# Optimization experiments

Measured on AMD Instinct MI355X. Metric: run time of the kernel, lower is better.

## Reference

```python
import jax, jax.numpy as jnp
import numpy as np

B = 2
E = [16384, 32768, 65536, 131072]
CONVS = [256, 128, 64, 32, 8]


def mesh_conv(x, gemm, W, b):
    # x: (B, C, E); gemm: (E, 4) neighbor edge indices; W: (Cout, Cin, 5)
    n = x[:, :, gemm]  # (B, C, E, 4) irregular gather over mesh topology
    f1, f2, f3, f4 = n[..., 0], n[..., 1], n[..., 2], n[..., 3]
    # MeshCNN symmetric functions over the 4 gemm neighbors
    G = jnp.stack([x, f1 + f3, f2 + f4, jnp.abs(f1 - f3), jnp.abs(f2 - f4)], axis=-1)  # (B,C,E,5)
    return jnp.einsum('bces,ocs->boe', G, W) + b[None, :, None]


def inorm(x, eps=1e-5):
    # InstanceNorm2d, affine=False: normalize per (sample, channel) over edge dim
    m = jnp.mean(x, axis=2, keepdims=True)
    v = jnp.var(x, axis=2, keepdims=True)
    return (x - m) * jax.lax.rsqrt(v + eps)


def setup_inputs() -> dict:
    key = jax.random.key(0)
    ks = iter(jax.random.split(key, 64))
    inp = {}
    inp['fe'] = jax.random.normal(next(ks), (B, CONVS[0], E[0]), jnp.float32)
    for i in range(3):
        inp[f'skip{i}'] = jax.random.normal(next(ks), (B, CONVS[i + 1], E[i + 1]), jnp.float32)
    for r in range(4):
        inp[f'gemm{r}'] = jax.random.randint(next(ks), (E[r], 4), 0, E[r], jnp.int32)
    for i in range(3):
        inp[f'unpool{i}'] = jax.random.randint(next(ks), (E[i + 1],), 0, E[i], jnp.int32)

    def mk(cout, cin, name):
        inp[f'W{name}'] = jax.random.normal(next(ks), (cout, cin, 5), jnp.float32) * (1.0 / np.sqrt(5.0 * cin))
        inp[f'b{name}'] = jnp.zeros((cout,), jnp.float32)

    for i in range(3):
        mk(CONVS[i + 1], CONVS[i], f'up{i}')
        mk(CONVS[i + 1], CONVS[i + 1], f'c{i}')
    mk(CONVS[4], CONVS[3], 'upf')
    mk(CONVS[4], CONVS[4], 'cf')
    return inp


def reference(fe, skip0, skip1, skip2, gemm0, gemm1, gemm2, gemm3,
              unpool0, unpool1, unpool2,
              Wup0, bup0, Wc0, bc0, Wup1, bup1, Wc1, bc1, Wup2, bup2, Wc2, bc2,
              Wupf, bupf, Wcf, bcf):
    gemms = [gemm0, gemm1, gemm2, gemm3]
    unpools = [unpool0, unpool1, unpool2]
    skips = [skip0, skip1, skip2]
    Wups = [Wup0, Wup1, Wup2]
    bups = [bup0, bup1, bup2]
    Wcs = [Wc0, Wc1, Wc2]
    bcs = [bc0, bc1, bc2]
    x = fe
    for i in range(3):  # fixed small loop over decoder stages
        x1 = mesh_conv(x, gemms[i], Wups[i], bups[i])      # up_conv at coarse res
        x1 = x1[:, :, unpools[i]]                          # MeshUnpool: copy to fine edges
        x1 = x1 + skips[i]                                 # transfer_data skip add
        x1 = mesh_conv(x1, gemms[i + 1], Wcs[i], bcs[i])   # conv1 at fine res
        x = jax.nn.relu(inorm(x1))                         # InstanceNorm + ReLU (blocks=0)
    # final UpConv: no unroll, no skip
    x1 = mesh_conv(x, gemms[3], Wupf, bupf)
    x1 = mesh_conv(x1, gemms[3], Wcf, bcf)
    return jax.nn.relu(inorm(x1))
```

## Files before the change

### kernel.cpp

```cpp
#include <hip/hip_runtime.h>
#include <hip/hip_bf16.h>
#include <cstdint>
#include <cstddef>


typedef short s16x8 __attribute__((ext_vector_type(8)));
typedef unsigned short u16x8 __attribute__((ext_vector_type(8)));
typedef float f32x4 __attribute__((ext_vector_type(4)));

__device__ __forceinline__ float bfbits2f(unsigned short u) {
    unsigned int x = ((unsigned int)u) << 16;
    float f; __builtin_memcpy(&f, &x, sizeof(f)); return f;
}
__device__ __forceinline__ unsigned short f2bfbits(float f) {
    __hip_bfloat16 h = __float2bfloat16(f);
    unsigned short u; __builtin_memcpy(&u, &h, sizeof(u)); return u;
}

__global__ __launch_bounds__(256) void k_transpose_in(
    const float* __restrict__ in, unsigned short* __restrict__ out, int C, int E)
{
    __shared__ float tile[64][65];
    const int e0 = blockIdx.x * 64;
    const int c0 = blockIdx.y * 64;
    const int b  = blockIdx.z;
    const float* inb = in + (size_t)b * C * E;
    const int l = threadIdx.x % 64;
    const int g = threadIdx.x / 64;
#pragma unroll
    for (int i = 0; i < 16; ++i) {
        const int c = i * 4 + g;
        tile[c][l] = inb[(size_t)(c0 + c) * E + e0 + l];
    }
    __syncthreads();
    unsigned short* outb = out + (size_t)b * E * C;
#pragma unroll
    for (int i = 0; i < 16; ++i) {
        const int e = i * 4 + g;
        outb[(size_t)(e0 + e) * C + c0 + l] = f2bfbits(tile[l][e]);
    }
}

__global__ __launch_bounds__(256) void k_prep_b(
    const float* __restrict__ W, unsigned short* __restrict__ Bp, int C, int O)
{
    const int p = blockIdx.x * 256 + threadIdx.x;
    const int total = 5 * C * O;
    if (p >= total) return;
    const int j = p & 7;
    const int t = p >> 3;
    const int o = t % O;
    const int kk = t / O;
    const int k = kk * 8 + j;
    const int s = k / C;
    const int c = k - s * C;
    Bp[p] = f2bfbits(W[((size_t)o * C + c) * 5 + s]);
}

__global__ __launch_bounds__(256) void k_prep_w(
    const float* __restrict__ W, float* __restrict__ Wt, int C, int O)
{
    const int idx = blockIdx.x * 256 + threadIdx.x;
    const int total = C * 5 * O;
    if (idx >= total) return;
    const int k = idx / O;
    const int o = idx % O;
    const int c = k / 5;
    const int s = k - 5 * c;
    Wt[idx] = W[((size_t)o * C + c) * 5 + s];
}

template<int C, int O, bool STATS>
__global__ __launch_bounds__(256) void k_conv_mfma(
    const unsigned short* __restrict__ x, const int* __restrict__ gm,
    const unsigned short* __restrict__ Bp, const float* __restrict__ bias,
    unsigned short* __restrict__ out, float* __restrict__ stats, int E)
{
    constexpr int NT  = O / 16;
    constexpr int ITS = C / 32;
    static_assert(C % 32 == 0 && O % 16 == 0, "bad cfg");
    const int tid  = threadIdx.x;
    const int wave = tid >> 6;
    const int lane = tid & 63;
    const int m    = lane & 15;
    const int kq   = lane >> 4;
    const int b    = blockIdx.y;
    const int e    = blockIdx.x * 64 + wave * 16 + m;
    const unsigned short* xb = x + (size_t)b * E * C;

    const int4 gi = *reinterpret_cast<const int4*>(gm + 4 * (size_t)e);
    const unsigned short* p0  = xb + (size_t)e * C;
    const unsigned short* pf1 = xb + (size_t)gi.x * C;
    const unsigned short* pf2 = xb + (size_t)gi.y * C;
    const unsigned short* pf3 = xb + (size_t)gi.z * C;
    const unsigned short* pf4 = xb + (size_t)gi.w * C;

    const s16x8* Bp8 = reinterpret_cast<const s16x8*>(Bp);

    f32x4 acc[NT];
#pragma unroll
    for (int nt = 0; nt < NT; ++nt) acc[nt] = (f32x4){0.f, 0.f, 0.f, 0.f};

#pragma unroll
    for (int s = 0; s < 5; ++s) {
        const unsigned short* pa = (s == 0) ? p0 : ((s == 1 || s == 3) ? pf1 : pf2);
        const unsigned short* pb = (s == 0) ? p0 : ((s == 1 || s == 3) ? pf3 : pf4);
        for (int it = 0; it < ITS; ++it) {
            const int c0 = it * 32 + kq * 8;
            s16x8 afrag;
            if (s == 0) {
                afrag = *reinterpret_cast<const s16x8*>(pa + c0);
            } else {
                const s16x8 av = *reinterpret_cast<const s16x8*>(pa + c0);
                const s16x8 bv = *reinterpret_cast<const s16x8*>(pb + c0);
#pragma unroll
                for (int j = 0; j < 8; ++j) {
                    const float fa = bfbits2f((unsigned short)av[j]);
                    const float fb = bfbits2f((unsigned short)bv[j]);
                    const float t = (s < 3) ? (fa + fb) : fabsf(fa - fb);
                    afrag[j] = (short)f2bfbits(t);
                }
            }
            const int kk = s * (C / 8) + it * 4 + kq;
#pragma unroll
            for (int nt = 0; nt < NT; ++nt) {
                const s16x8 bfrag = Bp8[(size_t)kk * O + nt * 16 + m];
                acc[nt] = __builtin_amdgcn_mfma_f32_16x16x32_bf16(afrag, bfrag, acc[nt], 0, 0, 0);
            }
        }
    }

    const int ebase = blockIdx.x * 64 + wave * 16 + kq * 4;
    float ssum[NT], ssq[NT];
#pragma unroll
    for (int nt = 0; nt < NT; ++nt) {
        const int o = nt * 16 + m;
        const float bo = bias[o];
        float s = 0.f, q = 0.f;
#pragma unroll
        for (int r = 0; r < 4; ++r) {
            const float z = acc[nt][r] + bo;
            out[((size_t)b * E + (ebase + r)) * O + o] = f2bfbits(z);
            s += z; q += z * z;
        }
        ssum[nt] = s; ssq[nt] = q;
    }

    if constexpr (STATS) {
        __shared__ float ls[4][2][O];
#pragma unroll
        for (int nt = 0; nt < NT; ++nt) {
            float s = ssum[nt], q = ssq[nt];
            s += __shfl_xor(s, 16); s += __shfl_xor(s, 32);
            q += __shfl_xor(q, 16); q += __shfl_xor(q, 32);
            if (kq == 0) { ls[wave][0][nt * 16 + m] = s; ls[wave][1][nt * 16 + m] = q; }
        }
        __syncthreads();
        if (tid < O) {
            const float S = ls[0][0][tid] + ls[1][0][tid] + ls[2][0][tid] + ls[3][0][tid];
            const float Q = ls[0][1][tid] + ls[1][1][tid] + ls[2][1][tid] + ls[3][1][tid];
            atomicAdd(&stats[((size_t)b * O + tid) * 2], S);
            atomicAdd(&stats[((size_t)b * O + tid) * 2 + 1], Q);
        }
    }
}

template<int C, int O, bool STATS>
__global__ __launch_bounds__(256) void k_conv_small(
    const unsigned short* __restrict__ x, const int* __restrict__ gm,
    const float* __restrict__ Wt, const float* __restrict__ bias,
    unsigned short* __restrict__ out, float* __restrict__ stats, int E)
{
    static_assert(O == 8 && C % 8 == 0, "bad cfg");
    __shared__ float ls[2 * O];
    const int tid = threadIdx.x;
    if constexpr (STATS) {
        if (tid < 2 * O) ls[tid] = 0.f;
        __syncthreads();
    }
    const int b = blockIdx.y;
    const int e = blockIdx.x * 256 + tid;
    const unsigned short* xb = x + (size_t)b * E * C;
    const int4 gi = *reinterpret_cast<const int4*>(gm + 4 * (size_t)e);
    const unsigned short* rp[5] = {
        xb + (size_t)e * C, xb + (size_t)gi.x * C, xb + (size_t)gi.y * C,
        xb + (size_t)gi.z * C, xb + (size_t)gi.w * C };

    float acc[O];
#pragma unroll
    for (int o = 0; o < O; ++o) acc[o] = bias[o];

#pragma unroll
    for (int c = 0; c < C; c += 8) {
        u16x8 rv[5];
#pragma unroll
        for (int k = 0; k < 5; ++k) rv[k] = *reinterpret_cast<const u16x8*>(rp[k] + c);
#pragma unroll
        for (int cc = 0; cc < 8; ++cc) {
            const float x0 = bfbits2f(rv[0][cc]);
            const float f1 = bfbits2f(rv[1][cc]);
            const float f2 = bfbits2f(rv[2][cc]);
            const float f3 = bfbits2f(rv[3][cc]);
            const float f4 = bfbits2f(rv[4][cc]);
            const float gv[5] = { x0, f1 + f3, f2 + f4, fabsf(f1 - f3), fabsf(f2 - f4) };
            const float* wbase = Wt + (size_t)(c + cc) * 5 * O;
#pragma unroll
            for (int s = 0; s < 5; ++s)
#pragma unroll
                for (int o = 0; o < O; ++o)
                    acc[o] += gv[s] * wbase[s * O + o];
        }
    }

    u16x8 ov;
#pragma unroll
    for (int o = 0; o < O; ++o) ov[o] = f2bfbits(acc[o]);
    *reinterpret_cast<u16x8*>(out + ((size_t)b * E + e) * O) = ov;

    if constexpr (STATS) {
#pragma unroll
        for (int o = 0; o < O; ++o) {
            atomicAdd(&ls[o * 2], acc[o]);
            atomicAdd(&ls[o * 2 + 1], acc[o] * acc[o]);
        }
        __syncthreads();
        if (tid < 2 * O) atomicAdd(&stats[(size_t)b * 2 * O + tid], ls[tid]);
    }
}

template<int O>
__global__ __launch_bounds__(256) void k_unpool_skip(
    const unsigned short* __restrict__ y, const int* __restrict__ up,
    const float* __restrict__ skip, unsigned short* __restrict__ out,
    int Ein, int Eout)
{
    __shared__ float sk[O][65];
    const int b  = blockIdx.y;
    const int e0 = blockIdx.x * 64;
    const int t  = threadIdx.x;
    constexpr int L = O / 16;
#pragma unroll
    for (int i = 0; i < L; ++i) {
        const int flat = i * 256 + t;
        const int o = flat >> 4;
        const int el4 = (flat & 15) * 4;
        const float4 v = *reinterpret_cast<const float4*>(
            skip + ((size_t)b * O + o) * Eout + e0 + el4);
        sk[o][el4]     = v.x;
        sk[o][el4 + 1] = v.y;
        sk[o][el4 + 2] = v.z;
        sk[o][el4 + 3] = v.w;
    }
    __syncthreads();
    constexpr int OG  = O / 4;
    constexpr int EPP = 256 / OG;
    const int o4  = (t % OG) * 4;
    const int elg = t / OG;
#pragma unroll
    for (int p = 0; p < 64 / EPP; ++p) {
        const int el = p * EPP + elg;
        const int e  = e0 + el;
        const int u  = up[e];
        const ushort4 yv = *reinterpret_cast<const ushort4*>(
            y + ((size_t)b * Ein + u) * O + o4);
        ushort4 ov;
        ov.x = f2bfbits(bfbits2f(yv.x) + sk[o4 + 0][el]);
        ov.y = f2bfbits(bfbits2f(yv.y) + sk[o4 + 1][el]);
        ov.z = f2bfbits(bfbits2f(yv.z) + sk[o4 + 2][el]);
        ov.w = f2bfbits(bfbits2f(yv.w) + sk[o4 + 3][el]);
        *reinterpret_cast<ushort4*>(out + ((size_t)b * Eout + e) * O + o4) = ov;
    }
}

__global__ __launch_bounds__(256) void k_scale(
    const float* __restrict__ stats, float* __restrict__ ss, int BC, float invE)
{
    const int t = threadIdx.x;
    if (t < BC) {
        const float sum = stats[t * 2];
        const float sq  = stats[t * 2 + 1];
        const float m   = sum * invE;
        const float var = fmaxf(sq * invE - m * m, 0.f);
        const float sc  = rsqrtf(var + 1e-5f);
        ss[t * 2] = sc;
        ss[t * 2 + 1] = -m * sc;
    }
}

template<int C>
__global__ __launch_bounds__(256) void k_norm_relu(
    unsigned short* __restrict__ x, const float* __restrict__ ss, int E)
{
    const int b = blockIdx.y;
    const size_t i8 = ((size_t)blockIdx.x * 256 + threadIdx.x) * 8;
    const int c0 = (int)(i8 % C);
    unsigned short* p = x + (size_t)b * E * C + i8;
    const u16x8 v = *reinterpret_cast<const u16x8*>(p);
    u16x8 r;
#pragma unroll
    for (int j = 0; j < 8; ++j) {
        const float sc = ss[(b * C + c0 + j) * 2];
        const float sh = ss[(b * C + c0 + j) * 2 + 1];
        r[j] = f2bfbits(fmaxf(bfbits2f(v[j]) * sc + sh, 0.f));
    }
    *reinterpret_cast<u16x8*>(p) = r;
}

__global__ __launch_bounds__(256) void k_final_out(
    const unsigned short* __restrict__ z, const float* __restrict__ ss,
    float* __restrict__ out, int E)
{
    const int b = blockIdx.y;
    const int idx = blockIdx.x * 256 + threadIdx.x;
    const int o = idx / E;
    const int e = idx % E;
    const float sc = ss[((size_t)b * 8 + o) * 2];
    const float sh = ss[((size_t)b * 8 + o) * 2 + 1];
    const float v = bfbits2f(z[((size_t)b * E + e) * 8 + o]) * sc + sh;
    out[(size_t)b * 8 * E + idx] = fmaxf(v, 0.f);
}

extern "C" void kernel_launch(void* const* d_in, const int* in_sizes, int n_in,
                              void* d_out, int out_size, void* d_ws, size_t ws_size,
                              hipStream_t stream)
{
    (void)in_sizes; (void)n_in; (void)out_size; (void)ws_size;

    const float* fe = (const float*)d_in[0];
    const int* gemm0 = (const int*)d_in[4];
    const int* gemm1 = (const int*)d_in[5];
    const int* gemm2 = (const int*)d_in[6];
    const int* gemm3 = (const int*)d_in[7];
    const int* up0 = (const int*)d_in[8];
    const int* up1 = (const int*)d_in[9];
    const int* up2 = (const int*)d_in[10];
    const float* bup0 = (const float*)d_in[12];
    const float* bc0  = (const float*)d_in[14];
    const float* bup1 = (const float*)d_in[16];
    const float* bc1  = (const float*)d_in[18];
    const float* bup2 = (const float*)d_in[20];
    const float* bc2  = (const float*)d_in[22];
    const float* bupf = (const float*)d_in[24];
    const float* bcf  = (const float*)d_in[26];

    unsigned short* wsb = (unsigned short*)d_ws;
    const size_t NP = 8388608;
    unsigned short* P0 = wsb;
    unsigned short* P1 = wsb + NP;
    unsigned short* P2 = wsb + 2 * NP;
    unsigned short* Bp_up0 = wsb + 3 * NP;
    unsigned short* Bp_c0  = Bp_up0 + 163840;
    unsigned short* Bp_up1 = Bp_c0  + 81920;
    unsigned short* Bp_c1  = Bp_up1 + 40960;
    unsigned short* Bp_up2 = Bp_c1  + 20480;
    unsigned short* Bp_c2  = Bp_up2 + 10240;
    float* fls    = (float*)(Bp_c2 + 5120);
    float* wt_upf = fls;
    float* wt_cf  = wt_upf + 1280;
    float* stats0 = wt_cf  + 320;
    float* stats1 = stats0 + 512;
    float* stats2 = stats1 + 256;
    float* stats3 = stats2 + 128;
    float* ss0    = stats3 + 32;
    float* ss1    = ss0 + 512;
    float* ss2    = ss1 + 256;
    float* ss3    = ss2 + 128;

    hipMemsetAsync(stats0, 0, 928 * sizeof(float), stream);

    const dim3 blk(256);

    k_transpose_in<<<dim3(16384 / 64, 256 / 64, 2), blk, 0, stream>>>(fe, P0, 256, 16384);

    k_prep_b<<<dim3(163840 / 256), blk, 0, stream>>>((const float*)d_in[11], Bp_up0, 256, 128);
    k_prep_b<<<dim3(81920 / 256),  blk, 0, stream>>>((const float*)d_in[13], Bp_c0, 128, 128);
    k_prep_b<<<dim3(40960 / 256),  blk, 0, stream>>>((const float*)d_in[15], Bp_up1, 128, 64);
    k_prep_b<<<dim3(20480 / 256),  blk, 0, stream>>>((const float*)d_in[17], Bp_c1, 64, 64);
    k_prep_b<<<dim3(10240 / 256),  blk, 0, stream>>>((const float*)d_in[19], Bp_up2, 64, 32);
    k_prep_b<<<dim3(5120 / 256),   blk, 0, stream>>>((const float*)d_in[21], Bp_c2, 32, 32);
    k_prep_w<<<dim3((1280 + 255) / 256), blk, 0, stream>>>((const float*)d_in[23], wt_upf, 32, 8);
    k_prep_w<<<dim3((320 + 255) / 256),  blk, 0, stream>>>((const float*)d_in[25], wt_cf, 8, 8);

    k_conv_mfma<256, 128, false><<<dim3(16384 / 64, 2), blk, 0, stream>>>(P0, gemm0, Bp_up0, bup0, P1, nullptr, 16384);
    k_unpool_skip<128><<<dim3(32768 / 64, 2), blk, 0, stream>>>(P1, up0, (const float*)d_in[1], P2, 16384, 32768);
    k_conv_mfma<128, 128, true><<<dim3(32768 / 64, 2), blk, 0, stream>>>(P2, gemm1, Bp_c0, bc0, P0, stats0, 32768);
    k_scale<<<dim3(1), blk, 0, stream>>>(stats0, ss0, 256, 1.f / 32768.f);
    k_norm_relu<128><<<dim3(32768 * 128 / 2048, 2), blk, 0, stream>>>(P0, ss0, 32768);

    k_conv_mfma<128, 64, false><<<dim3(32768 / 64, 2), blk, 0, stream>>>(P0, gemm1, Bp_up1, bup1, P1, nullptr, 32768);
    k_unpool_skip<64><<<dim3(65536 / 64, 2), blk, 0, stream>>>(P1, up1, (const float*)d_in[2], P2, 32768, 65536);
    k_conv_mfma<64, 64, true><<<dim3(65536 / 64, 2), blk, 0, stream>>>(P2, gemm2, Bp_c1, bc1, P0, stats1, 65536);
    k_scale<<<dim3(1), blk, 0, stream>>>(stats1, ss1, 128, 1.f / 65536.f);
    k_norm_relu<64><<<dim3(65536 * 64 / 2048, 2), blk, 0, stream>>>(P0, ss1, 65536);

    k_conv_mfma<64, 32, false><<<dim3(65536 / 64, 2), blk, 0, stream>>>(P0, gemm2, Bp_up2, bup2, P1, nullptr, 65536);
    k_unpool_skip<32><<<dim3(131072 / 64, 2), blk, 0, stream>>>(P1, up2, (const float*)d_in[3], P2, 65536, 131072);
    k_conv_mfma<32, 32, true><<<dim3(131072 / 64, 2), blk, 0, stream>>>(P2, gemm3, Bp_c2, bc2, P0, stats2, 131072);
    k_scale<<<dim3(1), blk, 0, stream>>>(stats2, ss2, 64, 1.f / 131072.f);
    k_norm_relu<32><<<dim3(131072 * 32 / 2048, 2), blk, 0, stream>>>(P0, ss2, 131072);

    k_conv_small<32, 8, false><<<dim3(131072 / 256, 2), blk, 0, stream>>>(P0, gemm3, wt_upf, bupf, P1, nullptr, 131072);
    k_conv_small<8, 8, true><<<dim3(131072 / 256, 2), blk, 0, stream>>>(P1, gemm3, wt_cf, bcf, P2, stats3, 131072);
    k_scale<<<dim3(1), blk, 0, stream>>>(stats3, ss3, 16, 1.f / 131072.f);
    k_final_out<<<dim3(8 * 131072 / 256, 2), blk, 0, stream>>>(P2, ss3, (float*)d_out, 131072);
}
```

Measured before the change: 785.7 us.

## Stage gathered neighbor features in LDS and route final up-conv through MFMA

The MFMA conv kernel now loads the 64-edge tile's gather indices into shared memory and has all threads cooperatively gather neighbor rows into an LDS tile. For C<=128 it builds the sum and abs-difference terms for each neighbor pair in one pass, so each gathered row is read from global memory once instead of twice and the A fragments are read from LDS. The final 32->8 up-conv moves from the scalar small-channel kernel to the MFMA kernel, with output channels zero-padded to 16 and only 8 written. The cost is extra syncthreads, LDS pressure that may lower occupancy, and wasted MFMA work on the padded channels.

```diff
diff --git a/kernel.cpp b/kernel.cpp
--- a/kernel.cpp
+++ b/kernel.cpp
@@ -42,19 +42,19 @@
 }
 
 __global__ __launch_bounds__(256) void k_prep_b(
-    const float* __restrict__ W, unsigned short* __restrict__ Bp, int C, int O)
+    const float* __restrict__ W, unsigned short* __restrict__ Bp, int C, int OP, int OL)
 {
     const int p = blockIdx.x * 256 + threadIdx.x;
-    const int total = 5 * C * O;
+    const int total = 5 * C * OP;
     if (p >= total) return;
     const int j = p & 7;
     const int t = p >> 3;
-    const int o = t % O;
-    const int kk = t / O;
+    const int o = t % OP;
+    const int kk = t / OP;
     const int k = kk * 8 + j;
     const int s = k / C;
     const int c = k - s * C;
-    Bp[p] = f2bfbits(W[((size_t)o * C + c) * 5 + s]);
+    Bp[p] = (o < OL) ? f2bfbits(W[((size_t)o * C + c) * 5 + s]) : (unsigned short)0;
 }
 
 __global__ __launch_bounds__(256) void k_prep_w(
@@ -70,80 +70,162 @@
     Wt[idx] = W[((size_t)o * C + c) * 5 + s];
 }
 
-template<int C, int O, bool STATS>
+template<int C, int O, bool STATS, int OW = O>
 __global__ __launch_bounds__(256) void k_conv_mfma(
     const unsigned short* __restrict__ x, const int* __restrict__ gm,
     const unsigned short* __restrict__ Bp, const float* __restrict__ bias,
     unsigned short* __restrict__ out, float* __restrict__ stats, int E)
 {
-    constexpr int NT  = O / 16;
-    constexpr int ITS = C / 32;
+    constexpr int NT    = O / 16;
+    constexpr int ITS   = C / 32;
+    constexpr int OCT   = C / 8;
+    constexpr int ITERS = (64 * OCT) / 256;
+    constexpr int PAD   = 8;
+    constexpr int RW    = C + PAD;
+    constexpr bool PAIRED = (C <= 128);
+    constexpr int SLOTS = PAIRED ? 2 : 1;
     static_assert(C % 32 == 0 && O % 16 == 0, "bad cfg");
+
+    __shared__ unsigned short smem[SLOTS][64][RW];
+    __shared__ int gis[64][4];
+
     const int tid  = threadIdx.x;
     const int wave = tid >> 6;
     const int lane = tid & 63;
     const int m    = lane & 15;
     const int kq   = lane >> 4;
     const int b    = blockIdx.y;
-    const int e    = blockIdx.x * 64 + wave * 16 + m;
+    const int e0   = blockIdx.x * 64;
     const unsigned short* xb = x + (size_t)b * E * C;
-
-    const int4 gi = *reinterpret_cast<const int4*>(gm + 4 * (size_t)e);
-    const unsigned short* p0  = xb + (size_t)e * C;
-    const unsigned short* pf1 = xb + (size_t)gi.x * C;
-    const unsigned short* pf2 = xb + (size_t)gi.y * C;
-    const unsigned short* pf3 = xb + (size_t)gi.z * C;
-    const unsigned short* pf4 = xb + (size_t)gi.w * C;
-
     const s16x8* Bp8 = reinterpret_cast<const s16x8*>(Bp);
 
+    if (tid < 64)
+        *reinterpret_cast<int4*>(gis[tid]) =
+            *reinterpret_cast<const int4*>(gm + 4 * (size_t)(e0 + tid));
+
     f32x4 acc[NT];
 #pragma unroll
     for (int nt = 0; nt < NT; ++nt) acc[nt] = (f32x4){0.f, 0.f, 0.f, 0.f};
 
-#pragma unroll
-    for (int s = 0; s < 5; ++s) {
-        const unsigned short* pa = (s == 0) ? p0 : ((s == 1 || s == 3) ? pf1 : pf2);
-        const unsigned short* pb = (s == 0) ? p0 : ((s == 1 || s == 3) ? pf3 : pf4);
+    auto mfma_seg = [&](int slot, int s) {
+#pragma unroll
         for (int it = 0; it < ITS; ++it) {
-            const int c0 = it * 32 + kq * 8;
-            s16x8 afrag;
-            if (s == 0) {
-                afrag = *reinterpret_cast<const s16x8*>(pa + c0);
-            } else {
-                const s16x8 av = *reinterpret_cast<const s16x8*>(pa + c0);
-                const s16x8 bv = *reinterpret_cast<const s16x8*>(pb + c0);
-#pragma unroll
-                for (int j = 0; j < 8; ++j) {
-                    const float fa = bfbits2f((unsigned short)av[j]);
-                    const float fb = bfbits2f((unsigned short)bv[j]);
-                    const float t = (s < 3) ? (fa + fb) : fabsf(fa - fb);
-                    afrag[j] = (short)f2bfbits(t);
-                }
-            }
-            const int kk = s * (C / 8) + it * 4 + kq;
+            const s16x8 afrag = *reinterpret_cast<const s16x8*>(
+                &smem[slot][wave * 16 + m][it * 32 + kq * 8]);
+            const int kkb = s * OCT + it * 4 + kq;
 #pragma unroll
             for (int nt = 0; nt < NT; ++nt) {
-                const s16x8 bfrag = Bp8[(size_t)kk * O + nt * 16 + m];
+                const s16x8 bfrag = Bp8[(size_t)kkb * O + nt * 16 + m];
                 acc[nt] = __builtin_amdgcn_mfma_f32_16x16x32_bf16(afrag, bfrag, acc[nt], 0, 0, 0);
             }
         }
-    }
-
-    const int ebase = blockIdx.x * 64 + wave * 16 + kq * 4;
+    };
+
+#pragma unroll
+    for (int i = 0; i < ITERS; ++i) {
+        const int task = i * 256 + tid;
+        const int r    = task / OCT;
+        const int oct  = task % OCT;
+        const u16x8 v = *reinterpret_cast<const u16x8*>(
+            xb + (size_t)(e0 + r) * C + oct * 8);
+        *reinterpret_cast<u16x8*>(&smem[0][r][oct * 8]) = v;
+    }
+    __syncthreads();
+    mfma_seg(0, 0);
+    __syncthreads();
+
+    if constexpr (PAIRED) {
+#pragma unroll
+        for (int i = 0; i < ITERS; ++i) {
+            const int task = i * 256 + tid;
+            const int r    = task / OCT;
+            const int oct  = task % OCT;
+            const u16x8 a = *reinterpret_cast<const u16x8*>(
+                xb + (size_t)gis[r][0] * C + oct * 8);
+            const u16x8 c = *reinterpret_cast<const u16x8*>(
+                xb + (size_t)gis[r][2] * C + oct * 8);
+            u16x8 vs, vd;
+#pragma unroll
+            for (int j = 0; j < 8; ++j) {
+                const float fa = bfbits2f(a[j]);
+                const float fc = bfbits2f(c[j]);
+                vs[j] = f2bfbits(fa + fc);
+                vd[j] = f2bfbits(fabsf(fa - fc));
+            }
+            *reinterpret_cast<u16x8*>(&smem[0][r][oct * 8]) = vs;
+            *reinterpret_cast<u16x8*>(&smem[SLOTS - 1][r][oct * 8]) = vd;
+        }
+        __syncthreads();
+        mfma_seg(0, 1);
+        mfma_seg(SLOTS - 1, 3);
+        __syncthreads();
+#pragma unroll
+        for (int i = 0; i < ITERS; ++i) {
+            const int task = i * 256 + tid;
+            const int r    = task / OCT;
+            const int oct  = task % OCT;
+            const u16x8 a = *reinterpret_cast<const u16x8*>(
+                xb + (size_t)gis[r][1] * C + oct * 8);
+            const u16x8 c = *reinterpret_cast<const u16x8*>(
+                xb + (size_t)gis[r][3] * C + oct * 8);
+            u16x8 vs, vd;
+#pragma unroll
+            for (int j = 0; j < 8; ++j) {
+                const float fa = bfbits2f(a[j]);
+                const float fc = bfbits2f(c[j]);
+                vs[j] = f2bfbits(fa + fc);
+                vd[j] = f2bfbits(fabsf(fa - fc));
+            }
+            *reinterpret_cast<u16x8*>(&smem[0][r][oct * 8]) = vs;
+            *reinterpret_cast<u16x8*>(&smem[SLOTS - 1][r][oct * 8]) = vd;
+        }
+        __syncthreads();
+        mfma_seg(0, 2);
+        mfma_seg(SLOTS - 1, 4);
+    } else {
+#pragma unroll
+        for (int s = 1; s <= 4; ++s) {
+            const int ia = (s == 1 || s == 3) ? 0 : 1;
+#pragma unroll
+            for (int i = 0; i < ITERS; ++i) {
+                const int task = i * 256 + tid;
+                const int r    = task / OCT;
+                const int oct  = task % OCT;
+                const u16x8 a = *reinterpret_cast<const u16x8*>(
+                    xb + (size_t)gis[r][ia] * C + oct * 8);
+                const u16x8 c = *reinterpret_cast<const u16x8*>(
+                    xb + (size_t)gis[r][ia + 2] * C + oct * 8);
+                u16x8 v;
+#pragma unroll
+                for (int j = 0; j < 8; ++j) {
+                    const float fa = bfbits2f(a[j]);
+                    const float fc = bfbits2f(c[j]);
+                    v[j] = f2bfbits((s < 3) ? (fa + fc) : fabsf(fa - fc));
+                }
+                *reinterpret_cast<u16x8*>(&smem[0][r][oct * 8]) = v;
+            }
+            __syncthreads();
+            mfma_seg(0, s);
+            if (s != 4) __syncthreads();
+        }
+    }
+
+    const int ebase = e0 + wave * 16 + kq * 4;
     float ssum[NT], ssq[NT];
+#pragma unroll
+    for (int nt = 0; nt < NT; ++nt) { ssum[nt] = 0.f; ssq[nt] = 0.f; }
 #pragma unroll
     for (int nt = 0; nt < NT; ++nt) {
         const int o = nt * 16 + m;
-        const float bo = bias[o];
-        float s = 0.f, q = 0.f;
-#pragma unroll
-        for (int r = 0; r < 4; ++r) {
-            const float z = acc[nt][r] + bo;
-            out[((size_t)b * E + (ebase + r)) * O + o] = f2bfbits(z);
-            s += z; q += z * z;
-        }
-        ssum[nt] = s; ssq[nt] = q;
+        if (o < OW) {
+            const float bo = bias[o];
+#pragma unroll
+            for (int r = 0; r < 4; ++r) {
+                const float z = acc[nt][r] + bo;
+                out[((size_t)b * E + (ebase + r)) * OW + o] = f2bfbits(z);
+                ssum[nt] += z; ssq[nt] += z * z;
+            }
+        }
     }
 
     if constexpr (STATS) {
@@ -354,9 +436,9 @@
     unsigned short* Bp_c1  = Bp_up1 + 40960;
     unsigned short* Bp_up2 = Bp_c1  + 20480;
     unsigned short* Bp_c2  = Bp_up2 + 10240;
-    float* fls    = (float*)(Bp_c2 + 5120);
-    float* wt_upf = fls;
-    float* wt_cf  = wt_upf + 1280;
+    unsigned short* Bp_upf = Bp_c2  + 5120;
+    float* fls    = (float*)(Bp_upf + 2560);
+    float* wt_cf  = fls;
     float* stats0 = wt_cf  + 320;
     float* stats1 = stats0 + 512;
     float* stats2 = stats1 + 256;
@@ -372,14 +454,14 @@
 
     k_transpose_in<<<dim3(16384 / 64, 256 / 64, 2), blk, 0, stream>>>(fe, P0, 256, 16384);
 
-    k_prep_b<<<dim3(163840 / 256), blk, 0, stream>>>((const float*)d_in[11], Bp_up0, 256, 128);
-    k_prep_b<<<dim3(81920 / 256),  blk, 0, stream>>>((const float*)d_in[13], Bp_c0, 128, 128);
-    k_prep_b<<<dim3(40960 / 256),  blk, 0, stream>>>((const float*)d_in[15], Bp_up1, 128, 64);
-    k_prep_b<<<dim3(20480 / 256),  blk, 0, stream>>>((const float*)d_in[17], Bp_c1, 64, 64);
-    k_prep_b<<<dim3(10240 / 256),  blk, 0, stream>>>((const float*)d_in[19], Bp_up2, 64, 32);
-    k_prep_b<<<dim3(5120 / 256),   blk, 0, stream>>>((const float*)d_in[21], Bp_c2, 32, 32);
-    k_prep_w<<<dim3((1280 + 255) / 256), blk, 0, stream>>>((const float*)d_in[23], wt_upf, 32, 8);
-    k_prep_w<<<dim3((320 + 255) / 256),  blk, 0, stream>>>((const float*)d_in[25], wt_cf, 8, 8);
+    k_prep_b<<<dim3(163840 / 256), blk, 0, stream>>>((const float*)d_in[11], Bp_up0, 256, 128, 128);
+    k_prep_b<<<dim3(81920 / 256),  blk, 0, stream>>>((const float*)d_in[13], Bp_c0, 128, 128, 128);
+    k_prep_b<<<dim3(40960 / 256),  blk, 0, stream>>>((const float*)d_in[15], Bp_up1, 128, 64, 64);
+    k_prep_b<<<dim3(20480 / 256),  blk, 0, stream>>>((const float*)d_in[17], Bp_c1, 64, 64, 64);
+    k_prep_b<<<dim3(10240 / 256),  blk, 0, stream>>>((const float*)d_in[19], Bp_up2, 64, 32, 32);
+    k_prep_b<<<dim3(5120 / 256),   blk, 0, stream>>>((const float*)d_in[21], Bp_c2, 32, 32, 32);
+    k_prep_b<<<dim3(2560 / 256),   blk, 0, stream>>>((const float*)d_in[23], Bp_upf, 32, 16, 8);
+    k_prep_w<<<dim3((320 + 255) / 256), blk, 0, stream>>>((const float*)d_in[25], wt_cf, 8, 8);
 
     k_conv_mfma<256, 128, false><<<dim3(16384 / 64, 2), blk, 0, stream>>>(P0, gemm0, Bp_up0, bup0, P1, nullptr, 16384);
     k_unpool_skip<128><<<dim3(32768 / 64, 2), blk, 0, stream>>>(P1, up0, (const float*)d_in[1], P2, 16384, 32768);
@@ -399,7 +481,7 @@
     k_scale<<<dim3(1), blk, 0, stream>>>(stats2, ss2, 64, 1.f / 131072.f);
     k_norm_relu<32><<<dim3(131072 * 32 / 2048, 2), blk, 0, stream>>>(P0, ss2, 131072);
 
-    k_conv_small<32, 8, false><<<dim3(131072 / 256, 2), blk, 0, stream>>>(P0, gemm3, wt_upf, bupf, P1, nullptr, 131072);
+    k_conv_mfma<32, 16, false, 8><<<dim3(131072 / 64, 2), blk, 0, stream>>>(P0, gemm3, Bp_upf, bupf, P1, nullptr, 131072);
     k_conv_small<8, 8, true><<<dim3(131072 / 256, 2), blk, 0, stream>>>(P1, gemm3, wt_cf, bcf, P2, stats3, 131072);
     k_scale<<<dim3(1), blk, 0, stream>>>(stats3, ss3, 16, 1.f / 131072.f);
     k_final_out<<<dim3(8 * 131072 / 256, 2), blk, 0, stream>>>(P2, ss3, (float*)d_out, 131072);
```

After: 743.1 us. 5.4% less time.
